# Performance work log

Measured on AMD Instinct MI355X. Metric: run time of the kernel, lower is better.

## Reference

```python
import jax, jax.numpy as jnp
import numpy as np

B, S, P, D_IN, D_MODEL = 8, 512, 8, 768, 1024
EPS = 1e-5


def setup_inputs() -> dict:
    key = jax.random.key(0)
    k1, k2, k3, k4 = jax.random.split(key, 4)
    param_vectors = jax.random.normal(k1, (B, S, P, D_IN), dtype=jnp.float32)
    num_params = jax.random.randint(k2, (B, S), 0, P + 1)  # 0..P valid params per position
    # Linear(768, d_model) params, torch default init: U(-1/sqrt(fan_in), 1/sqrt(fan_in))
    bound = 1.0 / np.sqrt(D_IN)
    W = jax.random.uniform(k3, (D_IN, D_MODEL), minval=-bound, maxval=bound, dtype=jnp.float32)
    b = jax.random.uniform(k4, (D_MODEL,), minval=-bound, maxval=bound, dtype=jnp.float32)
    gamma = jnp.ones((D_MODEL,), dtype=jnp.float32)
    beta = jnp.zeros((D_MODEL,), dtype=jnp.float32)
    return {"param_vectors": param_vectors, "num_params": num_params,
            "W": W, "b": b, "gamma": gamma, "beta": beta}


def reference(param_vectors, num_params, W, b, gamma, beta):
    # param_vectors: [B,S,P,768], num_params: [B,S] ints in [0,P]
    # One batched GEMM over all param vectors (replaces per-vector nn.Linear calls)
    emb = jnp.einsum('bspc,cd->bspd', param_vectors, W) + b  # [B,S,P,d_model]
    mask = (jnp.arange(P)[None, None, :] < num_params[:, :, None])  # [B,S,P]
    emb = emb * mask[..., None].astype(emb.dtype)
    cnt = num_params.astype(emb.dtype)[:, :, None]  # [B,S,1]
    pooled = emb.sum(axis=2) / jnp.maximum(cnt, 1.0)  # empty positions -> zeros
    # LayerNorm over last dim
    mu = pooled.mean(axis=-1, keepdims=True)
    var = jnp.mean(jnp.square(pooled - mu), axis=-1, keepdims=True)
    return (pooled - mu) * jax.lax.rsqrt(var + EPS) * gamma + beta
```

## Files before the change

kernel.cpp:

```cpp
#include <hip/hip_runtime.h>
#include <hip/hip_bf16.h>

typedef unsigned short u16;
typedef __bf16 bf16x8 __attribute__((ext_vector_type(8)));
typedef float f32x4 __attribute__((ext_vector_type(4)));

#define GLDS16(g, l)                                                           \
  __builtin_amdgcn_global_load_lds(                                            \
      (const __attribute__((address_space(1))) unsigned int*)(g),              \
      (__attribute__((address_space(3))) unsigned int*)(l), 16, 0, 0)

static __device__ __forceinline__ u16 f2bf(float f) {
  unsigned int u = __builtin_bit_cast(unsigned int, f);
  u = (u + 0x7fffu + ((u >> 16) & 1u)) >> 16;
  return (u16)u;
}

__global__ __launch_bounds__(256) void wcast_kernel(const float* __restrict__ W,
                                                    u16* __restrict__ Wt) {
  __shared__ float tile[32][33];
  const int n0 = blockIdx.x * 32;
  const int k0 = blockIdx.y * 32;
  const int t = threadIdx.x;
#pragma unroll
  for (int i = 0; i < 4; i++) {
    int idx = t + i * 256;
    int r = idx >> 5, c = idx & 31;
    tile[r][c] = W[(size_t)(k0 + r) * 1024 + n0 + c];
  }
  __syncthreads();
#pragma unroll
  for (int i = 0; i < 4; i++) {
    int idx = t + i * 256;
    int r = idx >> 5, c = idx & 31;
    Wt[(size_t)(n0 + r) * 768 + k0 + c] = f2bf(tile[c][r]);
  }
}

__global__ __launch_bounds__(192) void reduce_kernel(const float* __restrict__ pv,
                                                     const int* __restrict__ np,
                                                     u16* __restrict__ X) {
  const int pos = blockIdx.x;
  const int t = threadIdx.x;
  const int c = np[pos];
  const float4* base = (const float4*)(pv + (size_t)pos * 8 * 768);
  float4 acc = make_float4(0.f, 0.f, 0.f, 0.f);
  for (int p = 0; p < c; p++) {
    float4 v = base[p * 192 + t];
    acc.x += v.x; acc.y += v.y; acc.z += v.z; acc.w += v.w;
  }
  ushort4 o;
  o.x = f2bf(acc.x); o.y = f2bf(acc.y); o.z = f2bf(acc.z); o.w = f2bf(acc.w);
  ((ushort4*)(X + (size_t)pos * 768))[t] = o;
}

__global__ __launch_bounds__(256) void gemm_kernel(const u16* __restrict__ A,
                                                   const u16* __restrict__ Bt,
                                                   float* __restrict__ Y) {
  __shared__ __attribute__((aligned(16))) u16 As[128 * 32];
  __shared__ __attribute__((aligned(16))) u16 Bs[64 * 32];
  const int tid = threadIdx.x;
  const int wave = tid >> 6;
  const int lane = tid & 63;
  const int m0 = blockIdx.y * 128;
  const int n0 = blockIdx.x * 64;

  const int lr = lane >> 2;
  const int lk = (lane & 3) * 8;
  const u16* Ag0 = A + (size_t)(m0 + wave * 32 + lr) * 768 + lk;
  const u16* Ag1 = Ag0 + 16 * 768;
  const u16* Bg0 = Bt + (size_t)(n0 + wave * 16 + lr) * 768 + lk;
  u16* As0p = As + wave * 1024;
  u16* As1p = As0p + 512;
  u16* Bs0p = Bs + wave * 512;

  f32x4 zero = {0.f, 0.f, 0.f, 0.f};
  f32x4 acc[4][2];
#pragma unroll
  for (int i = 0; i < 4; i++)
#pragma unroll
    for (int j = 0; j < 2; j++) acc[i][j] = zero;

  const int wm = (wave >> 1) * 64;
  const int wn = (wave & 1) * 32;
  const int fm = lane & 15;
  const int fk = (lane >> 4) * 8;

  for (int k0 = 0; k0 < 768; k0 += 32) {
    __syncthreads();
    GLDS16(Ag0 + k0, As0p);
    GLDS16(Ag1 + k0, As1p);
    GLDS16(Bg0 + k0, Bs0p);
    __syncthreads();

    bf16x8 af[4], bfrag[2];
#pragma unroll
    for (int i = 0; i < 4; i++)
      af[i] = *(const bf16x8*)&As[(wm + i * 16 + fm) * 32 + fk];
#pragma unroll
    for (int j = 0; j < 2; j++)
      bfrag[j] = *(const bf16x8*)&Bs[(wn + j * 16 + fm) * 32 + fk];
#pragma unroll
    for (int i = 0; i < 4; i++)
#pragma unroll
      for (int j = 0; j < 2; j++)
        acc[i][j] = __builtin_amdgcn_mfma_f32_16x16x32_bf16(af[i], bfrag[j],
                                                            acc[i][j], 0, 0, 0);
  }

  const int cq = (lane >> 4) * 4;
#pragma unroll
  for (int i = 0; i < 4; i++) {
    int rbase = m0 + wm + i * 16 + cq;
#pragma unroll
    for (int j = 0; j < 2; j++) {
      int col = n0 + wn + j * 16 + fm;
#pragma unroll
      for (int r = 0; r < 4; r++)
        Y[(size_t)(rbase + r) * 1024 + col] = acc[i][j][r];
    }
  }
}

__global__ __launch_bounds__(256) void ln_kernel(const float* __restrict__ Y,
                                                 const int* __restrict__ np,
                                                 const float* __restrict__ b,
                                                 const float* __restrict__ gamma,
                                                 const float* __restrict__ beta,
                                                 float* __restrict__ out) {
  const int row = blockIdx.x;
  const int t = threadIdx.x;
  const int c = np[row];
  const float inv = c > 0 ? 1.0f / (float)c : 0.0f;
  const float bs = c > 0 ? 1.0f : 0.0f;

  float4 y = ((const float4*)(Y + (size_t)row * 1024))[t];
  float4 bb = ((const float4*)b)[t];
  float4 p;
  p.x = y.x * inv + bb.x * bs;
  p.y = y.y * inv + bb.y * bs;
  p.z = y.z * inv + bb.z * bs;
  p.w = y.w * inv + bb.w * bs;

  float s = p.x + p.y + p.z + p.w;
  float s2 = p.x * p.x + p.y * p.y + p.z * p.z + p.w * p.w;
#pragma unroll
  for (int off = 32; off > 0; off >>= 1) {
    s += __shfl_down(s, off);
    s2 += __shfl_down(s2, off);
  }
  __shared__ float red_s[4], red_s2[4];
  const int wave = t >> 6, lane = t & 63;
  if (lane == 0) { red_s[wave] = s; red_s2[wave] = s2; }
  __syncthreads();
  float ts = red_s[0] + red_s[1] + red_s[2] + red_s[3];
  float ts2 = red_s2[0] + red_s2[1] + red_s2[2] + red_s2[3];
  const float mu = ts * (1.0f / 1024.0f);
  float var = ts2 * (1.0f / 1024.0f) - mu * mu;
  const float rstd = rsqrtf(var + 1e-5f);

  float4 g = ((const float4*)gamma)[t];
  float4 be = ((const float4*)beta)[t];
  float4 o;
  o.x = (p.x - mu) * rstd * g.x + be.x;
  o.y = (p.y - mu) * rstd * g.y + be.y;
  o.z = (p.z - mu) * rstd * g.z + be.z;
  o.w = (p.w - mu) * rstd * g.w + be.w;
  ((float4*)(out + (size_t)row * 1024))[t] = o;
}

extern "C" void kernel_launch(void* const* d_in, const int* in_sizes, int n_in,
                              void* d_out, int out_size, void* d_ws,
                              size_t ws_size, hipStream_t stream) {
  const float* pv = (const float*)d_in[0];
  const int* np = (const int*)d_in[1];
  const float* W = (const float*)d_in[2];
  const float* b = (const float*)d_in[3];
  const float* gamma = (const float*)d_in[4];
  const float* beta = (const float*)d_in[5];
  float* out = (float*)d_out;

  char* ws = (char*)d_ws;
  u16* Wt = (u16*)ws;
  u16* X = (u16*)(ws + 1572864);
  float* Y = (float*)(ws + 1572864 + 6291456);

  wcast_kernel<<<dim3(32, 24), 256, 0, stream>>>(W, Wt);
  reduce_kernel<<<4096, 192, 0, stream>>>(pv, np, X);
  gemm_kernel<<<dim3(16, 32), 256, 0, stream>>>(X, Wt, Y);
  ln_kernel<<<4096, 256, 0, stream>>>(Y, np, b, gamma, beta, out);
}
```

Before: 178.8 us.

## Double-buffer GEMM LDS loads, shrink M tile, store GEMM output as bf16

The GEMM now double-buffers its LDS tiles so the next K slice is fetched while the current one is multiplied, with one barrier per step instead of two. The M tile is halved to 64, which doubles the grid, and the loop is fully unrolled. The intermediate Y buffer becomes bf16 instead of fp32, cutting GEMM store traffic and LayerNorm read traffic, at the cost of extra rounding before normalization. The reduce kernel also software-prefetches the next param vector.

```diff
diff --git a/kernel.cpp b/kernel.cpp
--- a/kernel.cpp
+++ b/kernel.cpp
@@ -14,6 +14,9 @@
   unsigned int u = __builtin_bit_cast(unsigned int, f);
   u = (u + 0x7fffu + ((u >> 16) & 1u)) >> 16;
   return (u16)u;
+}
+static __device__ __forceinline__ float bf2f(u16 h) {
+  return __builtin_bit_cast(float, (unsigned int)h << 16);
 }
 
 __global__ __launch_bounds__(256) void wcast_kernel(const float* __restrict__ W,
@@ -45,8 +48,13 @@
   const int c = np[pos];
   const float4* base = (const float4*)(pv + (size_t)pos * 8 * 768);
   float4 acc = make_float4(0.f, 0.f, 0.f, 0.f);
-  for (int p = 0; p < c; p++) {
-    float4 v = base[p * 192 + t];
+  if (c > 0) {
+    float4 v = base[t];
+    for (int p = 1; p < c; p++) {
+      float4 nv = base[p * 192 + t];
+      acc.x += v.x; acc.y += v.y; acc.z += v.z; acc.w += v.w;
+      v = nv;
+    }
     acc.x += v.x; acc.y += v.y; acc.z += v.z; acc.w += v.w;
   }
   ushort4 o;
@@ -56,73 +64,73 @@
 
 __global__ __launch_bounds__(256) void gemm_kernel(const u16* __restrict__ A,
                                                    const u16* __restrict__ Bt,
-                                                   float* __restrict__ Y) {
-  __shared__ __attribute__((aligned(16))) u16 As[128 * 32];
-  __shared__ __attribute__((aligned(16))) u16 Bs[64 * 32];
+                                                   u16* __restrict__ Y) {
+  __shared__ __attribute__((aligned(16))) u16 As[2][64 * 32];
+  __shared__ __attribute__((aligned(16))) u16 Bs[2][64 * 32];
   const int tid = threadIdx.x;
   const int wave = tid >> 6;
   const int lane = tid & 63;
-  const int m0 = blockIdx.y * 128;
+  const int m0 = blockIdx.y * 64;
   const int n0 = blockIdx.x * 64;
 
   const int lr = lane >> 2;
   const int lk = (lane & 3) * 8;
-  const u16* Ag0 = A + (size_t)(m0 + wave * 32 + lr) * 768 + lk;
-  const u16* Ag1 = Ag0 + 16 * 768;
-  const u16* Bg0 = Bt + (size_t)(n0 + wave * 16 + lr) * 768 + lk;
-  u16* As0p = As + wave * 1024;
-  u16* As1p = As0p + 512;
-  u16* Bs0p = Bs + wave * 512;
+  const u16* Ag = A + (size_t)(m0 + wave * 16 + lr) * 768 + lk;
+  const u16* Bg = Bt + (size_t)(n0 + wave * 16 + lr) * 768 + lk;
+  const int lds_off = wave * 512;
 
   f32x4 zero = {0.f, 0.f, 0.f, 0.f};
-  f32x4 acc[4][2];
-#pragma unroll
-  for (int i = 0; i < 4; i++)
+  f32x4 acc[2][2];
+#pragma unroll
+  for (int i = 0; i < 2; i++)
 #pragma unroll
     for (int j = 0; j < 2; j++) acc[i][j] = zero;
 
-  const int wm = (wave >> 1) * 64;
+  const int wm = (wave >> 1) * 32;
   const int wn = (wave & 1) * 32;
   const int fm = lane & 15;
   const int fk = (lane >> 4) * 8;
 
-  for (int k0 = 0; k0 < 768; k0 += 32) {
+  GLDS16(Ag, &As[0][lds_off]);
+  GLDS16(Bg, &Bs[0][lds_off]);
+
+#pragma unroll
+  for (int i = 0; i < 24; i++) {
     __syncthreads();
-    GLDS16(Ag0 + k0, As0p);
-    GLDS16(Ag1 + k0, As1p);
-    GLDS16(Bg0 + k0, Bs0p);
-    __syncthreads();
-
-    bf16x8 af[4], bfrag[2];
-#pragma unroll
-    for (int i = 0; i < 4; i++)
-      af[i] = *(const bf16x8*)&As[(wm + i * 16 + fm) * 32 + fk];
+    if (i + 1 < 24) {
+      GLDS16(Ag + (i + 1) * 32, &As[(i + 1) & 1][lds_off]);
+      GLDS16(Bg + (i + 1) * 32, &Bs[(i + 1) & 1][lds_off]);
+    }
+    bf16x8 af[2], bfr[2];
+#pragma unroll
+    for (int ii = 0; ii < 2; ii++)
+      af[ii] = *(const bf16x8*)&As[i & 1][(wm + ii * 16 + fm) * 32 + fk];
 #pragma unroll
     for (int j = 0; j < 2; j++)
-      bfrag[j] = *(const bf16x8*)&Bs[(wn + j * 16 + fm) * 32 + fk];
-#pragma unroll
-    for (int i = 0; i < 4; i++)
+      bfr[j] = *(const bf16x8*)&Bs[i & 1][(wn + j * 16 + fm) * 32 + fk];
+#pragma unroll
+    for (int ii = 0; ii < 2; ii++)
 #pragma unroll
       for (int j = 0; j < 2; j++)
-        acc[i][j] = __builtin_amdgcn_mfma_f32_16x16x32_bf16(af[i], bfrag[j],
-                                                            acc[i][j], 0, 0, 0);
+        acc[ii][j] = __builtin_amdgcn_mfma_f32_16x16x32_bf16(af[ii], bfr[j],
+                                                             acc[ii][j], 0, 0, 0);
   }
 
   const int cq = (lane >> 4) * 4;
 #pragma unroll
-  for (int i = 0; i < 4; i++) {
-    int rbase = m0 + wm + i * 16 + cq;
+  for (int ii = 0; ii < 2; ii++) {
+    int rbase = m0 + wm + ii * 16 + cq;
 #pragma unroll
     for (int j = 0; j < 2; j++) {
       int col = n0 + wn + j * 16 + fm;
 #pragma unroll
       for (int r = 0; r < 4; r++)
-        Y[(size_t)(rbase + r) * 1024 + col] = acc[i][j][r];
+        Y[(size_t)(rbase + r) * 1024 + col] = f2bf(acc[ii][j][r]);
     }
   }
 }
 
-__global__ __launch_bounds__(256) void ln_kernel(const float* __restrict__ Y,
+__global__ __launch_bounds__(256) void ln_kernel(const u16* __restrict__ Y,
                                                  const int* __restrict__ np,
                                                  const float* __restrict__ b,
                                                  const float* __restrict__ gamma,
@@ -134,13 +142,13 @@
   const float inv = c > 0 ? 1.0f / (float)c : 0.0f;
   const float bs = c > 0 ? 1.0f : 0.0f;
 
-  float4 y = ((const float4*)(Y + (size_t)row * 1024))[t];
+  ushort4 yv = ((const ushort4*)(Y + (size_t)row * 1024))[t];
   float4 bb = ((const float4*)b)[t];
   float4 p;
-  p.x = y.x * inv + bb.x * bs;
-  p.y = y.y * inv + bb.y * bs;
-  p.z = y.z * inv + bb.z * bs;
-  p.w = y.w * inv + bb.w * bs;
+  p.x = bf2f(yv.x) * inv + bb.x * bs;
+  p.y = bf2f(yv.y) * inv + bb.y * bs;
+  p.z = bf2f(yv.z) * inv + bb.z * bs;
+  p.w = bf2f(yv.w) * inv + bb.w * bs;
 
   float s = p.x + p.y + p.z + p.w;
   float s2 = p.x * p.x + p.y * p.y + p.z * p.z + p.w * p.w;
@@ -183,10 +191,10 @@
   char* ws = (char*)d_ws;
   u16* Wt = (u16*)ws;
   u16* X = (u16*)(ws + 1572864);
-  float* Y = (float*)(ws + 1572864 + 6291456);
+  u16* Y = (u16*)(ws + 1572864 + 6291456);
 
   wcast_kernel<<<dim3(32, 24), 256, 0, stream>>>(W, Wt);
   reduce_kernel<<<4096, 192, 0, stream>>>(pv, np, X);
-  gemm_kernel<<<dim3(16, 32), 256, 0, stream>>>(X, Wt, Y);
+  gemm_kernel<<<dim3(16, 64), 256, 0, stream>>>(X, Wt, Y);
   ln_kernel<<<4096, 256, 0, stream>>>(Y, np, b, gamma, beta, out);
 }
```

New measurement: 178.7 us. Within noise of the previous version (-0.0%).
